# Optimization experiments

Hardware: AMD Instinct MI355X
Metric: run time of the kernel (lower is better)

Reference implementation:

```python
import jax, jax.numpy as jnp
import numpy as np

KS = 7       # t_kernel_size
PAD = 3      # t_padding
IN_DIM = 64
D_K = 64
D_V = 64


def setup_inputs() -> dict:
    key = jax.random.key(0)
    ks = jax.random.split(key, 9)
    B, C, T, N = 8, IN_DIM, 128, 207
    scale = 1.0 / np.sqrt(C)
    return {
        "q": jax.random.normal(ks[0], (B, C, T, N), jnp.float32),
        "k": jax.random.normal(ks[1], (B, C, T, N), jnp.float32),
        "v": jax.random.normal(ks[2], (B, C, T, N), jnp.float32),
        "Wq": jax.random.normal(ks[3], (D_K, C), jnp.float32) * scale,
        "bq": jax.random.normal(ks[4], (D_K,), jnp.float32) * 0.01,
        "Wk": jax.random.normal(ks[5], (D_K, C), jnp.float32) * scale,
        "bk": jax.random.normal(ks[6], (D_K,), jnp.float32) * 0.01,
        "Wv": jax.random.normal(ks[7], (D_V, C), jnp.float32) * scale,
        "bv": jax.random.normal(ks[8], (D_V,), jnp.float32) * 0.01,
    }


def reference(q, k, v, Wq, bq, Wk, bk, Wv, bv):
    # 1x1 convs == per-position channel projections
    Q = jnp.einsum('bctn,oc->botn', q, Wq) + bq[None, :, None, None]
    K = jnp.einsum('bctn,oc->botn', k, Wk) + bk[None, :, None, None]
    V = jnp.einsum('bctn,oc->botn', v, Wv) + bv[None, :, None, None]
    # conv_k/conv_v zero-pad the time axis by PAD (padding=(t_padding, 0))
    Kp = jnp.pad(K, ((0, 0), (0, 0), (PAD, PAD), (0, 0)))
    Vp = jnp.pad(V, ((0, 0), (0, 0), (PAD, PAD), (0, 0)))
    T_in = q.shape[2]
    T_out = T_in + 2 * PAD - KS + 1  # stride=1, dilation=1 -> == T_in
    # unfold: sliding windows along time; [B, d, T_out, N, KS]
    Kw = jnp.stack([Kp[:, :, i:i + T_out, :] for i in range(KS)], axis=-1)
    Vw = jnp.stack([Vp[:, :, i:i + T_out, :] for i in range(KS)], axis=-1)
    # side='both': center-crop Q to T_out (offset == 0 here)
    off = (T_in - T_out) // 2
    Qs = Q[:, :, off:T_in - off, :]
    # per-channel windowed attention: scores [B, d, T_out, N, KS]
    scores = Qs[..., None] * Kw
    attn = jax.nn.softmax(scores, axis=-1)
    out = jnp.sum(attn * Vw, axis=-1)  # [B, d_v, T_out, N]
    return out
```

## Files before the change

kernel.cpp:

```cpp
#include <hip/hip_runtime.h>

typedef _Float16 half8 __attribute__((ext_vector_type(8)));
typedef float floatx4 __attribute__((ext_vector_type(4)));

#define B_DIM 8
#define C_DIM 64
#define T_DIM 128
#define N_DIM 207
#define O_DIM 64
#define CSTR  (T_DIM * N_DIM)

__global__ void pack_w(const float* __restrict__ Wq,
                       const float* __restrict__ Wk,
                       const float* __restrict__ Wv,
                       _Float16* __restrict__ ws)
{
    int i = threadIdx.x + blockIdx.x * blockDim.x;
    const int per = O_DIM * C_DIM;
    for (int m = i; m < 3 * per; m += blockDim.x * gridDim.x) {
        int arr = m / per, rem = m % per;
        const float* W = (arr == 0) ? Wq : (arr == 1) ? Wk : Wv;
        ws[m] = (_Float16)W[rem];
    }
}

__global__ __launch_bounds__(256, 3)
void attn_mfma(const float* __restrict__ q,
               const float* __restrict__ k,
               const float* __restrict__ v,
               const float* __restrict__ bq,
               const float* __restrict__ bk,
               const float* __restrict__ bv,
               const _Float16* __restrict__ wpk,
               float* __restrict__ out)
{
    __shared__ half8 xsf[2][6][64];

    const int tid  = threadIdx.x;
    const int lane = tid & 63;
    const int wv   = tid >> 6;
    const int nq   = lane & 15;
    const int qd   = lane >> 4;

    const int nb = blockIdx.x;
    const int tc = blockIdx.y;
    const int b  = blockIdx.z;

    const int t0 = tc * 16;
    const int o0 = wv * 16;
    const int n0 = nb * 16;

    const int sn  = tid & 15;
    const int cp2 = tid >> 4;
    const int wq  = cp2 >> 2;
    const int jp  = cp2 & 3;

    const int n_sc = min(n0 + sn, N_DIM - 1);
    const float* qb = q + (size_t)b * C_DIM * CSTR + n_sc;
    const float* kb = k + (size_t)b * C_DIM * CSTR + n_sc;
    const float* vb = v + (size_t)b * C_DIM * CSTR + n_sc;

    half8 af[3][2];
    #pragma unroll
    for (int arr = 0; arr < 3; ++arr)
        #pragma unroll
        for (int kk = 0; kk < 2; ++kk)
            af[arr][kk] = *(const half8*)(wpk + ((size_t)(arr * 64 + o0 + nq) * 64
                                                 + qd * 8 + kk * 32));

    float bq_r[4], bk_r[4], bv_r[4];
    #pragma unroll
    for (int j = 0; j < 4; ++j) {
        const int og = o0 + qd * 4 + j;
        bq_r[j] = bq[og]; bk_r[j] = bk[og]; bv_r[j] = bv[og];
    }

    float Kw[4][7], Vw[4][7], Qd4[4][4];
    #pragma unroll
    for (int j = 0; j < 4; ++j) {
        #pragma unroll
        for (int i = 0; i < 7; ++i) { Kw[j][i] = 0.f; Vw[j][i] = 0.f; }
        #pragma unroll
        for (int i = 0; i < 4; ++i) Qd4[j][i] = 0.f;
    }

    unsigned int* xw = (unsigned int*)&xsf[0][0][0];

    float pf[3][4];
    {
        const int tcl = max(t0 - 3, 0);
        const float* bases[3] = { qb, kb, vb };
        #pragma unroll
        for (int arr = 0; arr < 3; ++arr) {
            const float* p = bases[arr] + (size_t)tcl * N_DIM;
            pf[arr][0] = p[(2 * cp2    ) * CSTR];
            pf[arr][1] = p[(2 * cp2 + 1) * CSTR];
            pf[arr][2] = p[(2 * cp2 + 32) * CSTR];
            pf[arr][3] = p[(2 * cp2 + 33) * CSTR];
        }
    }

    for (int r = 0; r < 22; ++r) {
        const int buf = r & 1;

        #pragma unroll
        for (int arr = 0; arr < 3; ++arr) {
            auto p0 = __builtin_amdgcn_cvt_pkrtz(pf[arr][0], pf[arr][1]);
            auto p1 = __builtin_amdgcn_cvt_pkrtz(pf[arr][2], pf[arr][3]);
            xw[buf * 1536 + ((arr * 2 + 0) * 64 + wq * 16 + sn) * 4 + jp]
                = __builtin_bit_cast(unsigned int, p0);
            xw[buf * 1536 + ((arr * 2 + 1) * 64 + wq * 16 + sn) * 4 + jp]
                = __builtin_bit_cast(unsigned int, p1);
        }

        if (r < 21) {
            const int tg1 = t0 - 2 + r;
            const int tcl = min(max(tg1, 0), T_DIM - 1);
            const float* bases[3] = { qb, kb, vb };
            #pragma unroll
            for (int arr = 0; arr < 3; ++arr) {
                const float* p = bases[arr] + (size_t)tcl * N_DIM;
                pf[arr][0] = p[(2 * cp2    ) * CSTR];
                pf[arr][1] = p[(2 * cp2 + 1) * CSTR];
                pf[arr][2] = p[(2 * cp2 + 32) * CSTR];
                pf[arr][3] = p[(2 * cp2 + 33) * CSTR];
            }
        }

        __syncthreads();

        floatx4 aq = {0.f, 0.f, 0.f, 0.f};
        floatx4 ak = {0.f, 0.f, 0.f, 0.f};
        floatx4 av = {0.f, 0.f, 0.f, 0.f};
        aq = __builtin_amdgcn_mfma_f32_16x16x32_f16(af[0][0], xsf[buf][0][lane], aq, 0, 0, 0);
        aq = __builtin_amdgcn_mfma_f32_16x16x32_f16(af[0][1], xsf[buf][1][lane], aq, 0, 0, 0);
        ak = __builtin_amdgcn_mfma_f32_16x16x32_f16(af[1][0], xsf[buf][2][lane], ak, 0, 0, 0);
        ak = __builtin_amdgcn_mfma_f32_16x16x32_f16(af[1][1], xsf[buf][3][lane], ak, 0, 0, 0);
        av = __builtin_amdgcn_mfma_f32_16x16x32_f16(af[2][0], xsf[buf][4][lane], av, 0, 0, 0);
        av = __builtin_amdgcn_mfma_f32_16x16x32_f16(af[2][1], xsf[buf][5][lane], av, 0, 0, 0);

        const int tg = t0 - 3 + r;
        const bool rowv = (tg >= 0) && (tg < T_DIM);

        #pragma unroll
        for (int j = 0; j < 4; ++j) {
            #pragma unroll
            for (int i = 0; i < 6; ++i) { Kw[j][i] = Kw[j][i + 1]; Vw[j][i] = Vw[j][i + 1]; }
            #pragma unroll
            for (int i = 0; i < 3; ++i) Qd4[j][i] = Qd4[j][i + 1];
            Kw[j][6]  = rowv ? (ak[j] + bk_r[j]) : 0.f;
            Vw[j][6]  = rowv ? (av[j] + bv_r[j]) : 0.f;
            Qd4[j][3] = aq[j] + bq_r[j];
        }

        if (r >= 6) {
            const int to  = t0 + r - 6;
            const int n_g = n0 + nq;
            if (n_g < N_DIM) {
                #pragma unroll
                for (int j = 0; j < 4; ++j) {
                    const float qv = Qd4[j][0] * 1.44269504f;
                    float s[7];
                    #pragma unroll
                    for (int i = 0; i < 7; ++i) s[i] = qv * Kw[j][i];
                    float mx = s[0];
                    #pragma unroll
                    for (int i = 1; i < 7; ++i) mx = fmaxf(mx, s[i]);
                    float den = 0.f, num = 0.f;
                    #pragma unroll
                    for (int i = 0; i < 7; ++i) {
                        float e = exp2f(s[i] - mx);
                        den += e;
                        num = fmaf(e, Vw[j][i], num);
                    }
                    out[((size_t)(b * O_DIM + o0 + qd * 4 + j) * T_DIM + to) * N_DIM + n_g]
                        = num * __builtin_amdgcn_rcpf(den);
                }
            }
        }
    }
}

extern "C" void kernel_launch(void* const* d_in, const int* in_sizes, int n_in,
                              void* d_out, int out_size, void* d_ws, size_t ws_size,
                              hipStream_t stream)
{
    const float* q  = (const float*)d_in[0];
    const float* k  = (const float*)d_in[1];
    const float* v  = (const float*)d_in[2];
    const float* Wq = (const float*)d_in[3];
    const float* bq = (const float*)d_in[4];
    const float* Wk = (const float*)d_in[5];
    const float* bk = (const float*)d_in[6];
    const float* Wv = (const float*)d_in[7];
    const float* bv = (const float*)d_in[8];
    float* o = (float*)d_out;

    _Float16* ws_h = (_Float16*)d_ws;

    hipLaunchKernelGGL(pack_w, dim3(3), dim3(256), 0, stream, Wq, Wk, Wv, ws_h);

    dim3 grid(13, 8, B_DIM);
    dim3 block(256);
    hipLaunchKernelGGL(attn_mfma, grid, block, 0, stream,
                       q, k, v, bq, bk, bv, (const _Float16*)ws_h, o);
}
```

Measured before the change: 265.8 us.

## Widen blocks to 32 nodes, skip unused Q halo rows, double-buffer prefetch, swizzle blocks

Each block now covers 32 nodes with 512 threads (two 16-node halves across 8 waves), so node-tiling waste at the 207 boundary drops and there are fewer blocks (7x8x8). Q rows are only loaded, converted and projected for the 16 rows actually used, not the 6 halo rows. A two-register-set prefetch (pfA/pfB) with unrolled step pairs gives loads a full extra step of lead time. A block-index swizzle reorders block scheduling for locality. The risks are higher register pressure under launch_bounds(512,4) and doubled LDS use.

```diff
diff --git a/kernel.cpp b/kernel.cpp
--- a/kernel.cpp
+++ b/kernel.cpp
@@ -24,7 +24,109 @@
     }
 }
 
-__global__ __launch_bounds__(256, 3)
+
+#define LOADROW(pf, tg1, withQ)                                              \
+    {                                                                        \
+        const int tcl_ = min(max((tg1), 0), T_DIM - 1);                      \
+        if (withQ) {                                                         \
+            const float* p_ = qb + (size_t)tcl_ * N_DIM;                     \
+            pf[0][0] = p_[(2 * cp2     ) * CSTR];                            \
+            pf[0][1] = p_[(2 * cp2 +  1) * CSTR];                            \
+            pf[0][2] = p_[(2 * cp2 + 32) * CSTR];                            \
+            pf[0][3] = p_[(2 * cp2 + 33) * CSTR];                            \
+        }                                                                    \
+        {                                                                    \
+            const float* p_ = kb + (size_t)tcl_ * N_DIM;                     \
+            pf[1][0] = p_[(2 * cp2     ) * CSTR];                            \
+            pf[1][1] = p_[(2 * cp2 +  1) * CSTR];                            \
+            pf[1][2] = p_[(2 * cp2 + 32) * CSTR];                            \
+            pf[1][3] = p_[(2 * cp2 + 33) * CSTR];                            \
+        }                                                                    \
+        {                                                                    \
+            const float* p_ = vb + (size_t)tcl_ * N_DIM;                     \
+            pf[2][0] = p_[(2 * cp2     ) * CSTR];                            \
+            pf[2][1] = p_[(2 * cp2 +  1) * CSTR];                            \
+            pf[2][2] = p_[(2 * cp2 + 32) * CSTR];                            \
+            pf[2][3] = p_[(2 * cp2 + 33) * CSTR];                            \
+        }                                                                    \
+    }
+
+#define STEP(r, BUF, pf)                                                     \
+    {                                                                        \
+        const int  r_  = (r);                                                \
+        const bool qs_ = (r_ >= 3) && (r_ <= 18);                            \
+        {                                                                    \
+            auto pk0 = __builtin_amdgcn_cvt_pkrtz(pf[1][0], pf[1][1]);       \
+            auto pk1 = __builtin_amdgcn_cvt_pkrtz(pf[1][2], pf[1][3]);       \
+            auto pv0 = __builtin_amdgcn_cvt_pkrtz(pf[2][0], pf[2][1]);       \
+            auto pv1 = __builtin_amdgcn_cvt_pkrtz(pf[2][2], pf[2][3]);       \
+            xw[(BUF) * 3072 + 2 * 512 + sbase] = __builtin_bit_cast(unsigned int, pk0); \
+            xw[(BUF) * 3072 + 3 * 512 + sbase] = __builtin_bit_cast(unsigned int, pk1); \
+            xw[(BUF) * 3072 + 4 * 512 + sbase] = __builtin_bit_cast(unsigned int, pv0); \
+            xw[(BUF) * 3072 + 5 * 512 + sbase] = __builtin_bit_cast(unsigned int, pv1); \
+            if (qs_) {                                                       \
+                auto pq0 = __builtin_amdgcn_cvt_pkrtz(pf[0][0], pf[0][1]);   \
+                auto pq1 = __builtin_amdgcn_cvt_pkrtz(pf[0][2], pf[0][3]);   \
+                xw[(BUF) * 3072 + 0 * 512 + sbase] = __builtin_bit_cast(unsigned int, pq0); \
+                xw[(BUF) * 3072 + 1 * 512 + sbase] = __builtin_bit_cast(unsigned int, pq1); \
+            }                                                                \
+        }                                                                    \
+        if (r_ <= 19) {                                                      \
+            const bool wq_ = (r_ >= 1) && (r_ <= 16);                        \
+            LOADROW(pf, t0 - 1 + r_, wq_)                                    \
+        }                                                                    \
+        __syncthreads();                                                     \
+        floatx4 aq = {0.f, 0.f, 0.f, 0.f};                                   \
+        floatx4 ak = {0.f, 0.f, 0.f, 0.f};                                   \
+        floatx4 av = {0.f, 0.f, 0.f, 0.f};                                   \
+        ak = __builtin_amdgcn_mfma_f32_16x16x32_f16(af[1][0], xsf[BUF][ 4 + hn][lane], ak, 0, 0, 0); \
+        ak = __builtin_amdgcn_mfma_f32_16x16x32_f16(af[1][1], xsf[BUF][ 6 + hn][lane], ak, 0, 0, 0); \
+        av = __builtin_amdgcn_mfma_f32_16x16x32_f16(af[2][0], xsf[BUF][ 8 + hn][lane], av, 0, 0, 0); \
+        av = __builtin_amdgcn_mfma_f32_16x16x32_f16(af[2][1], xsf[BUF][10 + hn][lane], av, 0, 0, 0); \
+        if (qs_) {                                                           \
+            aq = __builtin_amdgcn_mfma_f32_16x16x32_f16(af[0][0], xsf[BUF][0 + hn][lane], aq, 0, 0, 0); \
+            aq = __builtin_amdgcn_mfma_f32_16x16x32_f16(af[0][1], xsf[BUF][2 + hn][lane], aq, 0, 0, 0); \
+        }                                                                    \
+        const int  tg_   = t0 - 3 + r_;                                      \
+        const bool rowv_ = (tg_ >= 0) && (tg_ < T_DIM);                      \
+        _Pragma("unroll")                                                    \
+        for (int j = 0; j < 4; ++j) {                                        \
+            _Pragma("unroll")                                                \
+            for (int i = 0; i < 6; ++i) { Kw[j][i] = Kw[j][i + 1]; Vw[j][i] = Vw[j][i + 1]; } \
+            _Pragma("unroll")                                                \
+            for (int i = 0; i < 3; ++i) Qd4[j][i] = Qd4[j][i + 1];           \
+            Kw[j][6]  = rowv_ ? (ak[j] + bk_r[j]) : 0.f;                     \
+            Vw[j][6]  = rowv_ ? (av[j] + bv_r[j]) : 0.f;                     \
+            Qd4[j][3] = aq[j] + bq_r[j];                                     \
+        }                                                                    \
+        if (r_ >= 6) {                                                       \
+            const int to_ = t0 + r_ - 6;                                     \
+            const int n_g = n0 + hn * 16 + nq;                               \
+            if (n_g < N_DIM) {                                               \
+                _Pragma("unroll")                                            \
+                for (int j = 0; j < 4; ++j) {                                \
+                    const float qv = Qd4[j][0] * 1.44269504f;                \
+                    float s[7];                                              \
+                    _Pragma("unroll")                                        \
+                    for (int i = 0; i < 7; ++i) s[i] = qv * Kw[j][i];        \
+                    float mx = s[0];                                         \
+                    _Pragma("unroll")                                        \
+                    for (int i = 1; i < 7; ++i) mx = fmaxf(mx, s[i]);        \
+                    float den = 0.f, num = 0.f;                              \
+                    _Pragma("unroll")                                        \
+                    for (int i = 0; i < 7; ++i) {                            \
+                        float e = exp2f(s[i] - mx);                          \
+                        den += e;                                            \
+                        num = fmaf(e, Vw[j][i], num);                        \
+                    }                                                        \
+                    out[((size_t)(b * O_DIM + o0 + qd * 4 + j) * T_DIM + to_) * N_DIM + n_g] \
+                        = num * __builtin_amdgcn_rcpf(den);                  \
+                }                                                            \
+            }                                                                \
+        }                                                                    \
+    }
+
+__global__ __launch_bounds__(512, 4)
 void attn_mfma(const float* __restrict__ q,
                const float* __restrict__ k,
                const float* __restrict__ v,
@@ -34,26 +136,30 @@
                const _Float16* __restrict__ wpk,
                float* __restrict__ out)
 {
-    __shared__ half8 xsf[2][6][64];
+    __shared__ half8 xsf[2][12][64];
 
     const int tid  = threadIdx.x;
     const int lane = tid & 63;
     const int wv   = tid >> 6;
+    const int hn   = wv >> 2;
     const int nq   = lane & 15;
     const int qd   = lane >> 4;
 
-    const int nb = blockIdx.x;
-    const int tc = blockIdx.y;
-    const int b  = blockIdx.z;
+    const int bid = blockIdx.x + 7 * (blockIdx.y + 8 * (int)blockIdx.z);
+    const int swz = (bid & 7) * 56 + (bid >> 3);
+    const int nb  = swz % 7;
+    const int tc  = (swz / 7) & 7;
+    const int b   = swz / 56;
 
     const int t0 = tc * 16;
-    const int o0 = wv * 16;
-    const int n0 = nb * 16;
-
-    const int sn  = tid & 15;
-    const int cp2 = tid >> 4;
-    const int wq  = cp2 >> 2;
-    const int jp  = cp2 & 3;
+    const int o0 = (wv & 3) * 16;
+    const int n0 = nb * 32;
+
+    const int sn    = tid & 31;
+    const int cp2   = tid >> 5;
+    const int wq    = cp2 >> 2;
+    const int jp    = cp2 & 3;
+    const int sbase = ((sn >> 4) * 64 + wq * 16 + (sn & 15)) * 4 + jp;
 
     const int n_sc = min(n0 + sn, N_DIM - 1);
     const float* qb = q + (size_t)b * C_DIM * CSTR + n_sc;
@@ -86,98 +192,18 @@
 
     unsigned int* xw = (unsigned int*)&xsf[0][0][0];
 
-    float pf[3][4];
-    {
-        const int tcl = max(t0 - 3, 0);
-        const float* bases[3] = { qb, kb, vb };
-        #pragma unroll
-        for (int arr = 0; arr < 3; ++arr) {
-            const float* p = bases[arr] + (size_t)tcl * N_DIM;
-            pf[arr][0] = p[(2 * cp2    ) * CSTR];
-            pf[arr][1] = p[(2 * cp2 + 1) * CSTR];
-            pf[arr][2] = p[(2 * cp2 + 32) * CSTR];
-            pf[arr][3] = p[(2 * cp2 + 33) * CSTR];
-        }
-    }
-
-    for (int r = 0; r < 22; ++r) {
-        const int buf = r & 1;
-
-        #pragma unroll
-        for (int arr = 0; arr < 3; ++arr) {
-            auto p0 = __builtin_amdgcn_cvt_pkrtz(pf[arr][0], pf[arr][1]);
-            auto p1 = __builtin_amdgcn_cvt_pkrtz(pf[arr][2], pf[arr][3]);
-            xw[buf * 1536 + ((arr * 2 + 0) * 64 + wq * 16 + sn) * 4 + jp]
-                = __builtin_bit_cast(unsigned int, p0);
-            xw[buf * 1536 + ((arr * 2 + 1) * 64 + wq * 16 + sn) * 4 + jp]
-                = __builtin_bit_cast(unsigned int, p1);
-        }
-
-        if (r < 21) {
-            const int tg1 = t0 - 2 + r;
-            const int tcl = min(max(tg1, 0), T_DIM - 1);
-            const float* bases[3] = { qb, kb, vb };
-            #pragma unroll
-            for (int arr = 0; arr < 3; ++arr) {
-                const float* p = bases[arr] + (size_t)tcl * N_DIM;
-                pf[arr][0] = p[(2 * cp2    ) * CSTR];
-                pf[arr][1] = p[(2 * cp2 + 1) * CSTR];
-                pf[arr][2] = p[(2 * cp2 + 32) * CSTR];
-                pf[arr][3] = p[(2 * cp2 + 33) * CSTR];
-            }
-        }
-
-        __syncthreads();
-
-        floatx4 aq = {0.f, 0.f, 0.f, 0.f};
-        floatx4 ak = {0.f, 0.f, 0.f, 0.f};
-        floatx4 av = {0.f, 0.f, 0.f, 0.f};
-        aq = __builtin_amdgcn_mfma_f32_16x16x32_f16(af[0][0], xsf[buf][0][lane], aq, 0, 0, 0);
-        aq = __builtin_amdgcn_mfma_f32_16x16x32_f16(af[0][1], xsf[buf][1][lane], aq, 0, 0, 0);
-        ak = __builtin_amdgcn_mfma_f32_16x16x32_f16(af[1][0], xsf[buf][2][lane], ak, 0, 0, 0);
-        ak = __builtin_amdgcn_mfma_f32_16x16x32_f16(af[1][1], xsf[buf][3][lane], ak, 0, 0, 0);
-        av = __builtin_amdgcn_mfma_f32_16x16x32_f16(af[2][0], xsf[buf][4][lane], av, 0, 0, 0);
-        av = __builtin_amdgcn_mfma_f32_16x16x32_f16(af[2][1], xsf[buf][5][lane], av, 0, 0, 0);
-
-        const int tg = t0 - 3 + r;
-        const bool rowv = (tg >= 0) && (tg < T_DIM);
-
-        #pragma unroll
-        for (int j = 0; j < 4; ++j) {
-            #pragma unroll
-            for (int i = 0; i < 6; ++i) { Kw[j][i] = Kw[j][i + 1]; Vw[j][i] = Vw[j][i + 1]; }
-            #pragma unroll
-            for (int i = 0; i < 3; ++i) Qd4[j][i] = Qd4[j][i + 1];
-            Kw[j][6]  = rowv ? (ak[j] + bk_r[j]) : 0.f;
-            Vw[j][6]  = rowv ? (av[j] + bv_r[j]) : 0.f;
-            Qd4[j][3] = aq[j] + bq_r[j];
-        }
-
-        if (r >= 6) {
-            const int to  = t0 + r - 6;
-            const int n_g = n0 + nq;
-            if (n_g < N_DIM) {
-                #pragma unroll
-                for (int j = 0; j < 4; ++j) {
-                    const float qv = Qd4[j][0] * 1.44269504f;
-                    float s[7];
-                    #pragma unroll
-                    for (int i = 0; i < 7; ++i) s[i] = qv * Kw[j][i];
-                    float mx = s[0];
-                    #pragma unroll
-                    for (int i = 1; i < 7; ++i) mx = fmaxf(mx, s[i]);
-                    float den = 0.f, num = 0.f;
-                    #pragma unroll
-                    for (int i = 0; i < 7; ++i) {
-                        float e = exp2f(s[i] - mx);
-                        den += e;
-                        num = fmaf(e, Vw[j][i], num);
-                    }
-                    out[((size_t)(b * O_DIM + o0 + qd * 4 + j) * T_DIM + to) * N_DIM + n_g]
-                        = num * __builtin_amdgcn_rcpf(den);
-                }
-            }
-        }
+    float pfA[3][4], pfB[3][4];
+    #pragma unroll
+    for (int a2 = 0; a2 < 3; ++a2)
+        #pragma unroll
+        for (int j = 0; j < 4; ++j) { pfA[a2][j] = 0.f; pfB[a2][j] = 0.f; }
+
+    LOADROW(pfA, t0 - 3, false)
+    LOADROW(pfB, t0 - 2, false)
+
+    for (int r2 = 0; r2 < 11; ++r2) {
+        STEP(2 * r2,     0, pfA);
+        STEP(2 * r2 + 1, 1, pfB);
     }
 }
 
@@ -200,8 +226,8 @@
 
     hipLaunchKernelGGL(pack_w, dim3(3), dim3(256), 0, stream, Wq, Wk, Wv, ws_h);
 
-    dim3 grid(13, 8, B_DIM);
-    dim3 block(256);
+    dim3 grid(7, 8, B_DIM);
+    dim3 block(512);
     hipLaunchKernelGGL(attn_mfma, grid, block, 0, stream,
                        q, k, v, bq, bk, bv, (const _Float16*)ws_h, o);
 }
```

Result: slower. 383.3 us (+44.2%).

## Stage inputs via async global-to-LDS loads with manual vmcnt double buffering

Applied to the files above, without the earlier changes.

Replaces register prefetch plus fp16 convert and LDS write with direct global_load_lds of fp32 inputs into a double-buffered shared tile. Fragments are converted to fp16 after reading from LDS, and explicit s_waitcnt vmcnt plus a single raw barrier per step replace __syncthreads. The aim is to cut VGPR pressure and staging instructions and overlap the next step's loads with compute. In exchange, LDS traffic doubles (fp32), and correctness depends on hand-tuned vmcnt counts that include output stores.

```diff
diff --git a/kernel.cpp b/kernel.cpp
--- a/kernel.cpp
+++ b/kernel.cpp
@@ -2,6 +2,8 @@
 
 typedef _Float16 half8 __attribute__((ext_vector_type(8)));
 typedef float floatx4 __attribute__((ext_vector_type(4)));
+typedef float f32x4 __attribute__((ext_vector_type(4)));
+typedef unsigned int uint4v __attribute__((ext_vector_type(4)));
 
 #define B_DIM 8
 #define C_DIM 64
@@ -24,6 +26,40 @@
     }
 }
 
+
+#define GLDS(gp_, lp_)                                                       \
+    __builtin_amdgcn_global_load_lds(                                        \
+        (const __attribute__((address_space(1))) void*)(gp_),                \
+        (__attribute__((address_space(3))) void*)(lp_), 4, 0, 0)
+
+#define STAGE(tg_, P_)                                                       \
+    {                                                                        \
+        const int tcl_  = min(max((tg_), 0), T_DIM - 1);                     \
+        const int toff_ = tcl_ * N_DIM;                                      \
+        _Pragma("unroll")                                                    \
+        for (int arr_ = 0; arr_ < 3; ++arr_) {                               \
+            const float* ab_ = (arr_ == 0) ? qb2 : (arr_ == 1) ? kb2 : vb2;  \
+            _Pragma("unroll")                                                \
+            for (int i_ = 0; i_ < 4; ++i_) {                                 \
+                GLDS(ab_ + toff_ + col_off[i_],                              \
+                     &xls[P_][arr_][wv * 4 + i_][0][0]);                     \
+            }                                                                \
+        }                                                                    \
+    }
+
+#define MKFRAG(P_, arr_, kk_, dst_)                                          \
+    {                                                                        \
+        const float* ch_ = &xls[P_][arr_][qd * 2 + (kk_) * 8][nq][0];        \
+        f32x4 A_ = *(const f32x4*)(ch_);                                     \
+        f32x4 B_ = *(const f32x4*)(ch_ + 64);                                \
+        uint4v t_;                                                           \
+        t_[0] = __builtin_bit_cast(unsigned int, __builtin_amdgcn_cvt_pkrtz(A_[0], A_[1])); \
+        t_[1] = __builtin_bit_cast(unsigned int, __builtin_amdgcn_cvt_pkrtz(A_[2], A_[3])); \
+        t_[2] = __builtin_bit_cast(unsigned int, __builtin_amdgcn_cvt_pkrtz(B_[0], B_[1])); \
+        t_[3] = __builtin_bit_cast(unsigned int, __builtin_amdgcn_cvt_pkrtz(B_[2], B_[3])); \
+        dst_ = __builtin_bit_cast(half8, t_);                                \
+    }
+
 __global__ __launch_bounds__(256, 3)
 void attn_mfma(const float* __restrict__ q,
                const float* __restrict__ k,
@@ -34,7 +70,7 @@
                const _Float16* __restrict__ wpk,
                float* __restrict__ out)
 {
-    __shared__ half8 xsf[2][6][64];
+    __shared__ __align__(16) float xls[2][3][16][16][4];
 
     const int tid  = threadIdx.x;
     const int lane = tid & 63;
@@ -50,15 +86,17 @@
     const int o0 = wv * 16;
     const int n0 = nb * 16;
 
-    const int sn  = tid & 15;
-    const int cp2 = tid >> 4;
-    const int wq  = cp2 >> 2;
-    const int jp  = cp2 & 3;
-
-    const int n_sc = min(n0 + sn, N_DIM - 1);
-    const float* qb = q + (size_t)b * C_DIM * CSTR + n_sc;
-    const float* kb = k + (size_t)b * C_DIM * CSTR + n_sc;
-    const float* vb = v + (size_t)b * C_DIM * CSTR + n_sc;
+    const int cl   = lane & 3;
+    const int nrow = lane >> 2;
+    const int n_cl = min(n0 + nrow, N_DIM - 1);
+    int col_off[4];
+    #pragma unroll
+    for (int i = 0; i < 4; ++i)
+        col_off[i] = ((wv * 4 + i) * 4 + cl) * CSTR + n_cl;
+
+    const float* qb2 = q + (size_t)b * C_DIM * CSTR;
+    const float* kb2 = k + (size_t)b * C_DIM * CSTR;
+    const float* vb2 = v + (size_t)b * C_DIM * CSTR;
 
     half8 af[3][2];
     #pragma unroll
@@ -84,62 +122,34 @@
         for (int i = 0; i < 4; ++i) Qd4[j][i] = 0.f;
     }
 
-    unsigned int* xw = (unsigned int*)&xsf[0][0][0];
-
-    float pf[3][4];
-    {
-        const int tcl = max(t0 - 3, 0);
-        const float* bases[3] = { qb, kb, vb };
-        #pragma unroll
-        for (int arr = 0; arr < 3; ++arr) {
-            const float* p = bases[arr] + (size_t)tcl * N_DIM;
-            pf[arr][0] = p[(2 * cp2    ) * CSTR];
-            pf[arr][1] = p[(2 * cp2 + 1) * CSTR];
-            pf[arr][2] = p[(2 * cp2 + 32) * CSTR];
-            pf[arr][3] = p[(2 * cp2 + 33) * CSTR];
-        }
-    }
+    STAGE(t0 - 3, 0);
 
     for (int r = 0; r < 22; ++r) {
-        const int buf = r & 1;
-
-        #pragma unroll
-        for (int arr = 0; arr < 3; ++arr) {
-            auto p0 = __builtin_amdgcn_cvt_pkrtz(pf[arr][0], pf[arr][1]);
-            auto p1 = __builtin_amdgcn_cvt_pkrtz(pf[arr][2], pf[arr][3]);
-            xw[buf * 1536 + ((arr * 2 + 0) * 64 + wq * 16 + sn) * 4 + jp]
-                = __builtin_bit_cast(unsigned int, p0);
-            xw[buf * 1536 + ((arr * 2 + 1) * 64 + wq * 16 + sn) * 4 + jp]
-                = __builtin_bit_cast(unsigned int, p1);
-        }
-
-        if (r < 21) {
-            const int tg1 = t0 - 2 + r;
-            const int tcl = min(max(tg1, 0), T_DIM - 1);
-            const float* bases[3] = { qb, kb, vb };
-            #pragma unroll
-            for (int arr = 0; arr < 3; ++arr) {
-                const float* p = bases[arr] + (size_t)tcl * N_DIM;
-                pf[arr][0] = p[(2 * cp2    ) * CSTR];
-                pf[arr][1] = p[(2 * cp2 + 1) * CSTR];
-                pf[arr][2] = p[(2 * cp2 + 32) * CSTR];
-                pf[arr][3] = p[(2 * cp2 + 33) * CSTR];
-            }
-        }
-
-        __syncthreads();
+        const int p = r & 1;
+
+        if (r <= 6) { asm volatile("s_waitcnt vmcnt(0)"); }
+        else        { asm volatile("s_waitcnt vmcnt(4)"); }
+        __builtin_amdgcn_s_barrier();
+        __builtin_amdgcn_sched_barrier(0);
+
+        if (r < 21) STAGE(t0 - 2 + r, 1 - p);
+
+        half8 fq0, fq1, fk0, fk1, fv0, fv1;
+        MKFRAG(p, 1, 0, fk0);  MKFRAG(p, 1, 1, fk1);
+        MKFRAG(p, 2, 0, fv0);  MKFRAG(p, 2, 1, fv1);
+        MKFRAG(p, 0, 0, fq0);  MKFRAG(p, 0, 1, fq1);
 
         floatx4 aq = {0.f, 0.f, 0.f, 0.f};
         floatx4 ak = {0.f, 0.f, 0.f, 0.f};
         floatx4 av = {0.f, 0.f, 0.f, 0.f};
-        aq = __builtin_amdgcn_mfma_f32_16x16x32_f16(af[0][0], xsf[buf][0][lane], aq, 0, 0, 0);
-        aq = __builtin_amdgcn_mfma_f32_16x16x32_f16(af[0][1], xsf[buf][1][lane], aq, 0, 0, 0);
-        ak = __builtin_amdgcn_mfma_f32_16x16x32_f16(af[1][0], xsf[buf][2][lane], ak, 0, 0, 0);
-        ak = __builtin_amdgcn_mfma_f32_16x16x32_f16(af[1][1], xsf[buf][3][lane], ak, 0, 0, 0);
-        av = __builtin_amdgcn_mfma_f32_16x16x32_f16(af[2][0], xsf[buf][4][lane], av, 0, 0, 0);
-        av = __builtin_amdgcn_mfma_f32_16x16x32_f16(af[2][1], xsf[buf][5][lane], av, 0, 0, 0);
-
-        const int tg = t0 - 3 + r;
+        ak = __builtin_amdgcn_mfma_f32_16x16x32_f16(af[1][0], fk0, ak, 0, 0, 0);
+        ak = __builtin_amdgcn_mfma_f32_16x16x32_f16(af[1][1], fk1, ak, 0, 0, 0);
+        av = __builtin_amdgcn_mfma_f32_16x16x32_f16(af[2][0], fv0, av, 0, 0, 0);
+        av = __builtin_amdgcn_mfma_f32_16x16x32_f16(af[2][1], fv1, av, 0, 0, 0);
+        aq = __builtin_amdgcn_mfma_f32_16x16x32_f16(af[0][0], fq0, aq, 0, 0, 0);
+        aq = __builtin_amdgcn_mfma_f32_16x16x32_f16(af[0][1], fq1, aq, 0, 0, 0);
+
+        const int  tg   = t0 - 3 + r;
         const bool rowv = (tg >= 0) && (tg < T_DIM);
 
         #pragma unroll
```

Result: slower. 271.8 us (+2.3%).
